# Kernel optimization log

Hardware: AMD Instinct MI355X
Metric: run time of the kernel (lower is better)

Reference implementation:

```python
import jax, jax.numpy as jnp
import numpy as np

D_MODEL = 1024
N_HEADS = 8
D_HEAD = 64
D_FF = 4096
LAMBDA_INIT = 0.8
EPS = 1e-5


def _ln(x, g, b):
    m = jnp.mean(x, axis=-1, keepdims=True)
    v = jnp.mean(jnp.square(x - m), axis=-1, keepdims=True)
    return (x - m) * jax.lax.rsqrt(v + EPS) * g + b


def setup_inputs() -> dict:
    key = jax.random.key(0)
    ks = jax.random.split(key, 24)
    D, H, Dh, F = D_MODEL, N_HEADS, D_HEAD, D_FF
    P = 2 * H * Dh  # projection width for q/k/v (== D here)
    s = lambda fan: 1.0 / np.sqrt(fan)
    inp = {
        'x': jax.random.normal(ks[0], (2, 2048, D), jnp.float32),
        'ln1_g': jnp.ones((D,), jnp.float32), 'ln1_b': jnp.zeros((D,), jnp.float32),
        'ln2_g': jnp.ones((D,), jnp.float32), 'ln2_b': jnp.zeros((D,), jnp.float32),
        'Wq': jax.random.normal(ks[1], (D, P), jnp.float32) * s(D), 'bq': jnp.zeros((P,), jnp.float32),
        'Wk': jax.random.normal(ks[2], (D, P), jnp.float32) * s(D), 'bk': jnp.zeros((P,), jnp.float32),
        'Wv': jax.random.normal(ks[3], (D, P), jnp.float32) * s(D), 'bv': jnp.zeros((P,), jnp.float32),
        'Wo': jax.random.normal(ks[4], (P, D), jnp.float32) * s(P), 'bo': jnp.zeros((D,), jnp.float32),
        'lq1': jax.random.normal(ks[5], (H, Dh), jnp.float32) * 0.1,
        'lk1': jax.random.normal(ks[6], (H, Dh), jnp.float32) * 0.1,
        'lq2': jax.random.normal(ks[7], (H, Dh), jnp.float32) * 0.1,
        'lk2': jax.random.normal(ks[8], (H, Dh), jnp.float32) * 0.1,
        'gn_w': jnp.ones((P,), jnp.float32), 'gn_b': jnp.zeros((P,), jnp.float32),
        'W1': jax.random.normal(ks[9], (D, F), jnp.float32) * s(D), 'b1': jnp.zeros((F,), jnp.float32),
        'Wg': jax.random.normal(ks[10], (F, F), jnp.float32) * s(F), 'bg': jnp.zeros((F,), jnp.float32),
        'W2': jax.random.normal(ks[11], (F, D), jnp.float32) * s(F), 'b2': jnp.zeros((D,), jnp.float32),
    }
    return inp


def reference(x, ln1_g, ln1_b, ln2_g, ln2_b, Wq, bq, Wk, bk, Wv, bv, Wo, bo,
              lq1, lk1, lq2, lk2, gn_w, gn_b, W1, b1, Wg, bg, W2, b2):
    B, S, D = x.shape
    H, Dh = N_HEADS, D_HEAD
    scale = 1.0 / np.sqrt(Dh)

    # --- differential attention sublayer (pre-norm) ---
    h = _ln(x, ln1_g, ln1_b)
    q = (h @ Wq + bq).reshape(B, S, H, 2, Dh)
    k = (h @ Wk + bk).reshape(B, S, H, 2, Dh)
    v = (h @ Wv + bv).reshape(B, S, H, 2 * Dh)

    A1 = jax.nn.softmax(jnp.einsum('bshd,bthd->bhst', q[..., 0, :], k[..., 0, :]) * scale, axis=-1)
    A2 = jax.nn.softmax(jnp.einsum('bshd,bthd->bhst', q[..., 1, :], k[..., 1, :]) * scale, axis=-1)

    lam = (jnp.exp(jnp.sum(lq1 * lk1, axis=-1))
           - jnp.exp(jnp.sum(lq2 * lk2, axis=-1)) + LAMBDA_INIT)  # [H]
    diff = A1 - lam[None, :, None, None] * A2                     # [B,H,S,S]
    o = jnp.einsum('bhst,bthe->bshe', diff, v)                    # [B,S,H,2*Dh]

    # headwise GroupNorm over the 2*Dh channels of each head
    mu = jnp.mean(o, axis=-1, keepdims=True)
    var = jnp.mean(jnp.square(o - mu), axis=-1, keepdims=True)
    o = (o - mu) * jax.lax.rsqrt(var + EPS)
    o = o * gn_w.reshape(H, 2 * Dh) + gn_b.reshape(H, 2 * Dh)
    o = o * (1.0 - LAMBDA_INIT)

    attn_out = o.reshape(B, S, 2 * H * Dh) @ Wo + bo
    x = x + attn_out

    # --- FFN sublayer: note source applies prenorm2 BEFORE residual split ---
    x = _ln(x, ln2_g, ln2_b)
    u = x @ W1 + b1
    u = u * jax.nn.silu(u @ Wg + bg)   # swiGLU gate
    return x + (u @ W2 + b2)
```

## Files before the change

kernel.cpp:

```cpp
#include <hip/hip_runtime.h>
#include <hip/hip_bf16.h>


typedef __attribute__((ext_vector_type(8))) __bf16 bf16x8;
typedef __attribute__((ext_vector_type(4))) float f32x4;

#define GAS __attribute__((address_space(1)))
#define LAS __attribute__((address_space(3)))

__device__ __forceinline__ unsigned short f2bf(float f) {
  unsigned u = __float_as_uint(f);
  u += 0x7fffu + ((u >> 16) & 1u);
  return (unsigned short)(u >> 16);
}
__device__ __forceinline__ float bf2f(unsigned short s) {
  return __uint_as_float(((unsigned)s) << 16);
}

__global__ __launch_bounds__(256)
void batched_transpose(const float* __restrict__ sWq, const float* __restrict__ sWk,
                       const float* __restrict__ sWv, const float* __restrict__ sWo,
                       const float* __restrict__ sW1, const float* __restrict__ sWg,
                       const float* __restrict__ sW2,
                       unsigned short* __restrict__ dstbase,
                       const float* __restrict__ bq, const float* __restrict__ bk,
                       const float* __restrict__ bv, float* __restrict__ bqkv,
                       float qscale) {
  const int id = blockIdx.x;
  if (id >= 7168) {
    const int i = (id - 7168) * 256 + threadIdx.x;
    if (i < 1024) bqkv[i] = bq[i] * qscale;
    else if (i < 2048) bqkv[i] = bk[i - 1024];
    else bqkv[i] = bv[i - 2048];
    return;
  }
  const float* W;
  int K, N, t;
  size_t doff;
  float scale = 1.0f;
  if (id < 256)       { W = sWq; K = 1024; N = 1024; t = id;        doff = 0;        scale = qscale; }
  else if (id < 512)  { W = sWk; K = 1024; N = 1024; t = id - 256;  doff = 1048576;  }
  else if (id < 768)  { W = sWv; K = 1024; N = 1024; t = id - 512;  doff = 2097152;  }
  else if (id < 1024) { W = sWo; K = 1024; N = 1024; t = id - 768;  doff = 3145728;  }
  else if (id < 2048) { W = sW1; K = 1024; N = 4096; t = id - 1024; doff = 4194304;  }
  else if (id < 6144) { W = sWg; K = 4096; N = 4096; t = id - 2048; doff = 8388608;  }
  else                { W = sW2; K = 4096; N = 1024; t = id - 6144; doff = 25165824; }
  unsigned short* WT = dstbase + doff;
  const int nx = N >> 6;
  const int n0 = (t % nx) * 64, k0 = (t / nx) * 64;

  __shared__ float tile[64][65];
  const int tr = threadIdx.x >> 4, tc = (threadIdx.x & 15) * 4;
#pragma unroll
  for (int i = 0; i < 4; ++i) {
    const float4 v = *(const float4*)&W[(size_t)(k0 + tr + i * 16) * N + n0 + tc];
    tile[tr + i * 16][tc + 0] = v.x;
    tile[tr + i * 16][tc + 1] = v.y;
    tile[tr + i * 16][tc + 2] = v.z;
    tile[tr + i * 16][tc + 3] = v.w;
  }
  __syncthreads();
#pragma unroll
  for (int i = 0; i < 4; ++i) {
    const int n = tr + i * 16;
    ushort4 o;
    o.x = f2bf(tile[tc + 0][n] * scale);
    o.y = f2bf(tile[tc + 1][n] * scale);
    o.z = f2bf(tile[tc + 2][n] * scale);
    o.w = f2bf(tile[tc + 3][n] * scale);
    *(ushort4*)&WT[(size_t)(n0 + n) * K + k0 + tc] = o;
  }
}

__global__ __launch_bounds__(256)
void kv_prep(const unsigned short* __restrict__ qkv, unsigned short* __restrict__ KP,
             unsigned short* __restrict__ VT) {
  __shared__ unsigned short tile[128][66];
  const int bh = blockIdx.y, b = bh >> 3, h = bh & 7;
  const int s0 = blockIdx.x * 64;
  const size_t inbase = (size_t)b * 2048 * 3072 + h * 128;
  const int tr = threadIdx.x >> 4, tc = (threadIdx.x & 15) * 8;
#pragma unroll
  for (int i = 0; i < 4; ++i) {
    const int s = s0 + tr + i * 16;
    *(uint4*)&KP[((size_t)bh * 2048 + s) * 128 + tc] =
        *(const uint4*)&qkv[inbase + (size_t)s * 3072 + 1024 + tc];
  }
#pragma unroll
  for (int i = 0; i < 4; ++i) {
    const int r = tr + i * 16;
    const uint4 v = *(const uint4*)&qkv[inbase + (size_t)(s0 + r) * 3072 + 2048 + tc];
    const unsigned short* pv = (const unsigned short*)&v;
#pragma unroll
    for (int jj = 0; jj < 8; ++jj) tile[tc + jj][r] = pv[jj];
  }
  __syncthreads();
  const int e = threadIdx.x >> 1, sh = (threadIdx.x & 1) * 32;
#pragma unroll
  for (int i = 0; i < 4; ++i) {
    ushort4 o0, o1;
    o0.x = tile[e][sh + i * 8 + 0]; o0.y = tile[e][sh + i * 8 + 1];
    o0.z = tile[e][sh + i * 8 + 2]; o0.w = tile[e][sh + i * 8 + 3];
    o1.x = tile[e][sh + i * 8 + 4]; o1.y = tile[e][sh + i * 8 + 5];
    o1.z = tile[e][sh + i * 8 + 6]; o1.w = tile[e][sh + i * 8 + 7];
    *(ushort4*)&VT[((size_t)bh * 128 + e) * 2048 + s0 + sh + i * 8] = o0;
    *(ushort4*)&VT[((size_t)bh * 128 + e) * 2048 + s0 + sh + i * 8 + 4] = o1;
  }
}

__global__ void lam_kernel(const float* __restrict__ lq1, const float* __restrict__ lk1,
                           const float* __restrict__ lq2, const float* __restrict__ lk2,
                           float* __restrict__ lam) {
  const int w = threadIdx.x >> 6, d = threadIdx.x & 63;
  float a = lq1[w * 64 + d] * lk1[w * 64 + d];
  float c = lq2[w * 64 + d] * lk2[w * 64 + d];
#pragma unroll
  for (int off = 32; off; off >>= 1) {
    a += __shfl_xor(a, off);
    c += __shfl_xor(c, off);
  }
  if (d == 0) lam[w] = __expf(a) - __expf(c) + 0.8f;
}

__global__ __launch_bounds__(256)
void ln_kernel(const float* __restrict__ x, const float* __restrict__ g,
               const float* __restrict__ bsh, unsigned short* __restrict__ obf) {
  __shared__ float red[16];
  const int row = blockIdx.x, tid = threadIdx.x;
  const float4 v = *(const float4*)&x[(size_t)row * 1024 + tid * 4];
  float s = v.x + v.y + v.z + v.w;
  float q = v.x * v.x + v.y * v.y + v.z * v.z + v.w * v.w;
#pragma unroll
  for (int off = 32; off; off >>= 1) {
    s += __shfl_xor(s, off);
    q += __shfl_xor(q, off);
  }
  if ((tid & 63) == 0) {
    red[tid >> 6] = s;
    red[8 + (tid >> 6)] = q;
  }
  __syncthreads();
  s = red[0] + red[1] + red[2] + red[3];
  q = red[8] + red[9] + red[10] + red[11];
  const float mean = s * (1.f / 1024.f);
  const float var = q * (1.f / 1024.f) - mean * mean;
  const float rstd = rsqrtf(var + 1e-5f);
  const float4 gg = *(const float4*)&g[tid * 4];
  const float4 bb = *(const float4*)&bsh[tid * 4];
  ushort4 o;
  o.x = f2bf((v.x - mean) * rstd * gg.x + bb.x);
  o.y = f2bf((v.y - mean) * rstd * gg.y + bb.y);
  o.z = f2bf((v.z - mean) * rstd * gg.z + bb.z);
  o.w = f2bf((v.w - mean) * rstd * gg.w + bb.w);
  *(ushort4*)&obf[(size_t)row * 1024 + tid * 4] = o;
}

template <int EPI>
__global__ __launch_bounds__(256)
void gemm128(const unsigned short* __restrict__ A,
             const unsigned short* __restrict__ BT,
             const float* __restrict__ bias,
             const float* __restrict__ resf,
             const unsigned short* __restrict__ resb,
             void* __restrict__ Cout, int M, int N, int K, float bscale) {
  __shared__ unsigned short lds[32768];
  const int tid = threadIdx.x;
  const int w = tid >> 6, ln = tid & 63, lg = ln >> 4, lc = ln & 15;
  const int wm = w >> 1, wn = w & 1;
  const int nwg = gridDim.x * gridDim.y;
  const int linear = blockIdx.y * gridDim.x + blockIdx.x;
  const int swzb = (linear & 7) * (nwg >> 3) + (linear >> 3);
  const int m0 = (swzb / gridDim.x) * 128, n0 = (swzb % gridDim.x) * 128;

  f32x4 acc[4][4];
#pragma unroll
  for (int i = 0; i < 4; ++i)
#pragma unroll
    for (int j = 0; j < 4; ++j) acc[i][j] = (f32x4)0.f;

  auto stage_half = [&](int tensor, int j, int hh) {
    const unsigned short* base = tensor ? BT : A;
    const int row0 = (tensor ? n0 : m0) + hh * 64;
    const int slot = tensor * 4 + (j & 1) * 2 + hh;
#pragma unroll
    for (int c = 0; c < 2; ++c) {
      const int chunk = w * 2 + c;
      const int L = chunk * 1024 + ln * 16;
      const int r = L >> 7, inner = L & 127;
      const char* src = (const char*)(base + (size_t)(row0 + r) * K + j * 64) +
                        (inner ^ ((r & 7) << 4));
      __builtin_amdgcn_global_load_lds((GAS void*)src,
          (LAS void*)((char*)lds + slot * 8192 + chunk * 1024), 16, 0, 0);
    }
  };
  auto read_a = [&](int j, int mf, int ks) -> bf16x8 {
    const int r = mf * 16 + lc;
    const int slot = (j & 1) * 2 + wm;
    const int cb = ks * 64 + lg * 16;
    return *(const bf16x8*)((const char*)lds + slot * 8192 + r * 128 +
                            (cb ^ ((r & 7) << 4)));
  };
  auto read_b = [&](int j, int nf, int ks) -> bf16x8 {
    const int R = wn * 64 + nf * 16 + lc;
    const int slot = 4 + (j & 1) * 2 + (R >> 6);
    const int r = R & 63;
    const int cb = ks * 64 + lg * 16;
    return *(const bf16x8*)((const char*)lds + slot * 8192 + r * 128 +
                            (cb ^ ((r & 7) << 4)));
  };

  const int nkt = K / 64;

  stage_half(0, 0, 0); stage_half(0, 0, 1);
  stage_half(1, 0, 0); stage_half(1, 0, 1);
  stage_half(1, 1, 0); stage_half(1, 1, 1);
  asm volatile("s_waitcnt vmcnt(0)" ::: "memory");
  __builtin_amdgcn_s_barrier();

  bf16x8 bfr[4][2];
  for (int it = 0; it < nkt / 2; ++it) {
    const int J = it * 2;
#pragma unroll
    for (int half = 0; half < 2; ++half) {
      const int jc = J + half;
#pragma unroll
      for (int q = 0; q < 2; ++q) {
        if (q == 0) {
#pragma unroll
          for (int nf = 0; nf < 4; ++nf)
#pragma unroll
            for (int ks = 0; ks < 2; ++ks) bfr[nf][ks] = read_b(jc, nf, ks);
        }
        bf16x8 afr[2][2];
#pragma unroll
        for (int mm = 0; mm < 2; ++mm)
#pragma unroll
          for (int ks = 0; ks < 2; ++ks) afr[mm][ks] = read_a(jc, q * 2 + mm, ks);
        if (half == 0) {
          if (q == 0) { stage_half(0, J + 1, 0); stage_half(0, J + 1, 1); }
          else if (J + 2 < nkt) { stage_half(1, J + 2, 0); stage_half(1, J + 2, 1); }
        } else {
          if (q == 0) { if (J + 2 < nkt) { stage_half(0, J + 2, 0); stage_half(0, J + 2, 1); } }
          else if (J + 3 < nkt) { stage_half(1, J + 3, 0); stage_half(1, J + 3, 1); }
        }
        __builtin_amdgcn_s_barrier();
        asm volatile("s_waitcnt lgkmcnt(0)" ::: "memory");
        __builtin_amdgcn_sched_barrier(0);
        __builtin_amdgcn_s_setprio(1);
#pragma unroll
        for (int mm = 0; mm < 2; ++mm)
#pragma unroll
          for (int nf = 0; nf < 4; ++nf)
#pragma unroll
            for (int ks = 0; ks < 2; ++ks)
              acc[q * 2 + mm][nf] = __builtin_amdgcn_mfma_f32_16x16x32_bf16(
                  afr[mm][ks], bfr[nf][ks], acc[q * 2 + mm][nf], 0, 0, 0);
        __builtin_amdgcn_s_setprio(0);
        if (q == 1) {
          if ((half == 0 && J + 2 < nkt) || (half == 1 && J + 3 < nkt))
            asm volatile("s_waitcnt vmcnt(4)" ::: "memory");
          else
            asm volatile("s_waitcnt vmcnt(0)" ::: "memory");
        }
        __builtin_amdgcn_s_barrier();
      }
    }
  }

#pragma unroll
  for (int mf = 0; mf < 4; ++mf) {
#pragma unroll
    for (int nf = 0; nf < 4; ++nf) {
      const int c = n0 + wn * 64 + nf * 16 + lc;
      const float bc = bias[c] * bscale;
#pragma unroll
      for (int jj = 0; jj < 4; ++jj) {
        const int r = m0 + wm * 64 + mf * 16 + lg * 4 + jj;
        const size_t idx = (size_t)r * N + c;
        const float v = acc[mf][nf][jj] + bc;
        if (EPI == 1) {
          ((float*)Cout)[idx] = resf[idx] + v;
        } else if (EPI == 2) {
          ((float*)Cout)[idx] = bf2f(resb[idx]) + v;
        } else {
          ((unsigned short*)Cout)[idx] = f2bf(v);
        }
      }
    }
  }
}

template <int EPI>
__global__ __launch_bounds__(512)
void gemm256(const unsigned short* __restrict__ A,
             const unsigned short* __restrict__ BT,
             const float* __restrict__ bias,
             const unsigned short* __restrict__ gate_u,
             unsigned short* __restrict__ Cout, int M, int N, int K) {
  __shared__ unsigned short lds[65536];
  const int tid = threadIdx.x;
  const int w = tid >> 6, ln = tid & 63, lg = ln >> 4, lc = ln & 15;
  const int wm = w >> 2, wn = w & 3;
  const int nwg = gridDim.x * gridDim.y;
  const int linear = blockIdx.y * gridDim.x + blockIdx.x;
  const int swzb = (linear & 7) * (nwg >> 3) + (linear >> 3);
  const int m0 = (swzb / gridDim.x) * 256, n0 = (swzb % gridDim.x) * 256;

  f32x4 acc[8][4];
#pragma unroll
  for (int i = 0; i < 8; ++i)
#pragma unroll
    for (int j = 0; j < 4; ++j) acc[i][j] = (f32x4)0.f;

  auto stage_half = [&](int tensor, int j, int hh) {
    const unsigned short* base = tensor ? BT : A;
    const int row0 = (tensor ? n0 : m0) + hh * 128;
    const int slot = tensor * 4 + (j & 1) * 2 + hh;
#pragma unroll
    for (int c = 0; c < 2; ++c) {
      const int chunk = w * 2 + c;
      const int L = chunk * 1024 + ln * 16;
      const int r = L >> 7, inner = L & 127;
      const char* src = (const char*)(base + (size_t)(row0 + r) * K + j * 64) +
                        (inner ^ ((r & 7) << 4));
      __builtin_amdgcn_global_load_lds((GAS void*)src,
          (LAS void*)((char*)lds + slot * 16384 + chunk * 1024), 16, 0, 0);
    }
  };
  auto read_a = [&](int j, int mf, int ks) -> bf16x8 {
    const int r = mf * 16 + lc;
    const int slot = (j & 1) * 2 + wm;
    const int cb = ks * 64 + lg * 16;
    return *(const bf16x8*)((const char*)lds + slot * 16384 + r * 128 +
                            (cb ^ ((r & 7) << 4)));
  };
  auto read_b = [&](int j, int nf, int ks) -> bf16x8 {
    const int R = wn * 64 + nf * 16 + lc;
    const int slot = 4 + (j & 1) * 2 + (R >> 7);
    const int r = R & 127;
    const int cb = ks * 64 + lg * 16;
    return *(const bf16x8*)((const char*)lds + slot * 16384 + r * 128 +
                            (cb ^ ((r & 7) << 4)));
  };

  const int nkt = K / 64;

  stage_half(0, 0, 0); stage_half(0, 0, 1);
  stage_half(1, 0, 0); stage_half(1, 0, 1);
  stage_half(1, 1, 0); stage_half(1, 1, 1);
  asm volatile("s_waitcnt vmcnt(0)" ::: "memory");
  __builtin_amdgcn_s_barrier();

  bf16x8 bfr[4][2];
  for (int it = 0; it < nkt / 2; ++it) {
    const int J = it * 2;
#pragma unroll
    for (int half = 0; half < 2; ++half) {
      const int jc = J + half;
#pragma unroll
      for (int q = 0; q < 4; ++q) {
        if (q == 0) {
#pragma unroll
          for (int nf = 0; nf < 4; ++nf)
#pragma unroll
            for (int ks = 0; ks < 2; ++ks) bfr[nf][ks] = read_b(jc, nf, ks);
        }
        bf16x8 afr[2][2];
#pragma unroll
        for (int mm = 0; mm < 2; ++mm)
#pragma unroll
          for (int ks = 0; ks < 2; ++ks) afr[mm][ks] = read_a(jc, q * 2 + mm, ks);
        if (half == 0) {
          if (q == 0) stage_half(0, J + 1, 0);
          if (q == 1) stage_half(0, J + 1, 1);
          if (q == 2 && J + 2 < nkt) stage_half(1, J + 2, 0);
          if (q == 3 && J + 2 < nkt) stage_half(1, J + 2, 1);
        } else {
          if (q == 0 && J + 2 < nkt) stage_half(0, J + 2, 0);
          if (q == 1 && J + 2 < nkt) stage_half(0, J + 2, 1);
          if (q == 2 && J + 3 < nkt) stage_half(1, J + 3, 0);
          if (q == 3 && J + 3 < nkt) stage_half(1, J + 3, 1);
        }
        __builtin_amdgcn_s_barrier();
        asm volatile("s_waitcnt lgkmcnt(0)" ::: "memory");
        __builtin_amdgcn_sched_barrier(0);
        __builtin_amdgcn_s_setprio(1);
#pragma unroll
        for (int mm = 0; mm < 2; ++mm)
#pragma unroll
          for (int nf = 0; nf < 4; ++nf)
#pragma unroll
            for (int ks = 0; ks < 2; ++ks)
              acc[q * 2 + mm][nf] = __builtin_amdgcn_mfma_f32_16x16x32_bf16(
                  afr[mm][ks], bfr[nf][ks], acc[q * 2 + mm][nf], 0, 0, 0);
        __builtin_amdgcn_s_setprio(0);
        if (q == 3) asm volatile("s_waitcnt vmcnt(4)" ::: "memory");
        __builtin_amdgcn_s_barrier();
      }
    }
  }

#pragma unroll
  for (int mf = 0; mf < 8; ++mf) {
#pragma unroll
    for (int nf = 0; nf < 4; ++nf) {
      const int c = n0 + wn * 64 + nf * 16 + lc;
      const float bc = bias[c];
#pragma unroll
      for (int jj = 0; jj < 4; ++jj) {
        const int r = m0 + wm * 128 + mf * 16 + lg * 4 + jj;
        const size_t idx = (size_t)r * N + c;
        const float v = acc[mf][nf][jj] + bc;
        if (EPI == 0) {
          Cout[idx] = f2bf(v);
        } else {
          const float uu = bf2f(gate_u[idx]);
          const float sw = v / (1.f + __expf(-v));
          Cout[idx] = f2bf(uu * sw);
        }
      }
    }
  }
}

__global__ __launch_bounds__(256)
void attn_kernel(const unsigned short* __restrict__ q,
                 const unsigned short* __restrict__ KP,
                 const unsigned short* __restrict__ VT,
                 const float* __restrict__ lam,
                 const float* __restrict__ gn_w, const float* __restrict__ gn_b,
                 unsigned short* __restrict__ o) {
  constexpr int S = 2048;
  constexpr int QS = 3072;
  __shared__ unsigned short k_tile[2][32 * 128];
  __shared__ unsigned short v_tile[2][128 * 32];
  __shared__ unsigned short p_lds[4][2][512];
  const int tid = threadIdx.x, w = tid >> 6, ln = tid & 63, lg = ln >> 4, lc = ln & 15;
  const int id = blockIdx.x;
  const int bh = (id & 7) + 8 * ((id >> 8) & 1);
  const int qt = (id >> 3) & 31;
  const int h = bh & 7, b = bh >> 3;
  const size_t chan = (size_t)b * S * QS + h * 128;
  const size_t ochan = (size_t)b * S * 1024 + h * 128;
  const size_t kpbase = (size_t)bh * S * 128;
  const size_t vtbase = (size_t)bh * 128 * S;
  const int qrow = qt * 64 + w * 16 + lc;

  bf16x8 qf[2][2];
#pragma unroll
  for (int p = 0; p < 2; ++p)
#pragma unroll
    for (int ks = 0; ks < 2; ++ks)
      qf[p][ks] = *(const bf16x8*)&q[chan + (size_t)qrow * QS + p * 64 + ks * 32 + lg * 8];

  f32x4 O[2][8];
#pragma unroll
  for (int p = 0; p < 2; ++p)
#pragma unroll
    for (int ef = 0; ef < 8; ++ef) O[p][ef] = (f32x4)0.f;
  float lsum[2][4];
#pragma unroll
  for (int p = 0; p < 2; ++p)
#pragma unroll
    for (int j = 0; j < 4; ++j) lsum[p][j] = 0.f;

  const int prd = ((lc * 64 + lg * 16) ^ ((lc & 7) << 4)) >> 1;

  auto stage = [&](int buf, int t0) {
#pragma unroll
    for (int c = 0; c < 2; ++c) {
      {
        const int L = (w * 2 + c) * 1024 + ln * 16;
        const int r = L >> 8, inner = L & 255;
        const char* src = (const char*)(KP + kpbase + (size_t)(t0 + r) * 128) +
                          (inner ^ ((r & 7) << 4));
        __builtin_amdgcn_global_load_lds((GAS void*)src,
            (LAS void*)((char*)&k_tile[buf][0] + (w * 2 + c) * 1024), 16, 0, 0);
      }
      {
        const int L = (w * 2 + c) * 1024 + ln * 16;
        const int e = L >> 6, inner = L & 63;
        const char* src = (const char*)(VT + vtbase + (size_t)e * S + t0) +
                          (inner ^ ((e & 3) << 4));
        __builtin_amdgcn_global_load_lds((GAS void*)src,
            (LAS void*)((char*)&v_tile[buf][0] + (w * 2 + c) * 1024), 16, 0, 0);
      }
    }
  };

  auto compute = [&](int buf) {
    const char* kb = (const char*)&k_tile[buf][0];
    const char* vb = (const char*)&v_tile[buf][0];
#pragma unroll
    for (int p = 0; p < 2; ++p) {
      bf16x8 kf[2][2];
#pragma unroll
      for (int tf = 0; tf < 2; ++tf) {
        const int r = tf * 16 + lc;
#pragma unroll
        for (int ks = 0; ks < 2; ++ks)
          kf[tf][ks] = *(const bf16x8*)(kb + r * 256 +
                          ((p * 128 + ks * 64 + lg * 16) ^ ((r & 7) << 4)));
      }
      f32x4 sfr[2];
      __builtin_amdgcn_s_setprio(1);
#pragma unroll
      for (int tf = 0; tf < 2; ++tf) {
        f32x4 acc = (f32x4)0.f;
#pragma unroll
        for (int ks = 0; ks < 2; ++ks)
          acc = __builtin_amdgcn_mfma_f32_16x16x32_bf16(qf[p][ks], kf[tf][ks], acc, 0, 0, 0);
        sfr[tf] = acc;
      }
      __builtin_amdgcn_s_setprio(0);
#pragma unroll
      for (int tf = 0; tf < 2; ++tf)
#pragma unroll
        for (int j = 0; j < 4; ++j) {
          const float e = __expf(sfr[tf][j]);
          lsum[p][j] += e;
          const int qq = lg * 4 + j;
          const int wi = ((qq * 64 + (tf * 16 + lc) * 2) ^ ((qq & 7) << 4)) >> 1;
          p_lds[w][p][wi] = f2bf(e);
        }
    }
    bf16x8 pa[2];
#pragma unroll
    for (int p = 0; p < 2; ++p)
      pa[p] = *(const bf16x8*)&p_lds[w][p][prd];
#pragma unroll
    for (int half = 0; half < 2; ++half) {
      bf16x8 vf[4];
#pragma unroll
      for (int ef = 0; ef < 4; ++ef) {
        const int e = (half * 4 + ef) * 16 + lc;
        vf[ef] = *(const bf16x8*)(vb + e * 64 + ((lg * 16) ^ ((e & 3) << 4)));
      }
      __builtin_amdgcn_s_setprio(1);
#pragma unroll
      for (int p = 0; p < 2; ++p)
#pragma unroll
        for (int ef = 0; ef < 4; ++ef)
          O[p][half * 4 + ef] = __builtin_amdgcn_mfma_f32_16x16x32_bf16(
              pa[p], vf[ef], O[p][half * 4 + ef], 0, 0, 0);
      __builtin_amdgcn_s_setprio(0);
    }
  };

  stage(0, 0);
  int cur = 0;
  for (int it = 0; it < 64; ++it) {
    if (it < 63) {
      stage(cur ^ 1, (it + 1) * 32);
      asm volatile("s_waitcnt vmcnt(4)" ::: "memory");
    } else {
      asm volatile("s_waitcnt vmcnt(0)" ::: "memory");
    }
    __builtin_amdgcn_s_barrier();
    compute(cur);
    __builtin_amdgcn_s_barrier();
    cur ^= 1;
  }

#pragma unroll
  for (int p = 0; p < 2; ++p)
#pragma unroll
    for (int j = 0; j < 4; ++j) {
      float s = lsum[p][j];
      s += __shfl_xor(s, 1);
      s += __shfl_xor(s, 2);
      s += __shfl_xor(s, 4);
      s += __shfl_xor(s, 8);
      lsum[p][j] = s;
    }
  const float lamh = lam[h];
#pragma unroll
  for (int j = 0; j < 4; ++j) {
    const float inv1 = 1.f / lsum[0][j];
    const float inv2 = lamh / lsum[1][j];
    float dv[8], sum = 0.f, sq = 0.f;
#pragma unroll
    for (int ef = 0; ef < 8; ++ef) {
      dv[ef] = O[0][ef][j] * inv1 - O[1][ef][j] * inv2;
      sum += dv[ef];
      sq += dv[ef] * dv[ef];
    }
    sum += __shfl_xor(sum, 1); sq += __shfl_xor(sq, 1);
    sum += __shfl_xor(sum, 2); sq += __shfl_xor(sq, 2);
    sum += __shfl_xor(sum, 4); sq += __shfl_xor(sq, 4);
    sum += __shfl_xor(sum, 8); sq += __shfl_xor(sq, 8);
    const float mean = sum * (1.f / 128.f);
    const float var = sq * (1.f / 128.f) - mean * mean;
    const float rstd = rsqrtf(var + 1e-5f);
    const int row = qt * 64 + w * 16 + lg * 4 + j;
#pragma unroll
    for (int ef = 0; ef < 8; ++ef) {
      const int e = ef * 16 + lc;
      const float val = (dv[ef] - mean) * rstd * gn_w[h * 128 + e] + gn_b[h * 128 + e];
      o[ochan + (size_t)row * 1024 + e] = f2bf(val * 0.2f);
    }
  }
}

extern "C" void kernel_launch(void* const* d_in, const int* in_sizes, int n_in,
                              void* d_out, int out_size, void* d_ws, size_t ws_size,
                              hipStream_t stream) {
  (void)in_sizes; (void)n_in; (void)out_size; (void)ws_size;
  const float* x    = (const float*)d_in[0];
  const float* ln1g = (const float*)d_in[1];
  const float* ln1b = (const float*)d_in[2];
  const float* ln2g = (const float*)d_in[3];
  const float* ln2b = (const float*)d_in[4];
  const float* Wq   = (const float*)d_in[5];
  const float* bq   = (const float*)d_in[6];
  const float* Wk   = (const float*)d_in[7];
  const float* bk   = (const float*)d_in[8];
  const float* Wv   = (const float*)d_in[9];
  const float* bv   = (const float*)d_in[10];
  const float* Wo   = (const float*)d_in[11];
  const float* bo   = (const float*)d_in[12];
  const float* lq1  = (const float*)d_in[13];
  const float* lk1  = (const float*)d_in[14];
  const float* lq2  = (const float*)d_in[15];
  const float* lk2  = (const float*)d_in[16];
  const float* gnw  = (const float*)d_in[17];
  const float* gnb  = (const float*)d_in[18];
  const float* W1   = (const float*)d_in[19];
  const float* b1   = (const float*)d_in[20];
  const float* Wg   = (const float*)d_in[21];
  const float* bg   = (const float*)d_in[22];
  const float* W2   = (const float*)d_in[23];
  const float* b2   = (const float*)d_in[24];

  const int B = 2, S = 2048, D = 1024, F = 4096;
  const int M = B * S;
  const float qscale = 0.125f;

  char* ws = (char*)d_ws;
  size_t off = 0;
  auto alloc = [&](size_t bytes) {
    char* p = ws + off;
    off += (bytes + 255) & ~(size_t)255;
    return p;
  };
  unsigned short* WqkvT = (unsigned short*)alloc((size_t)3 * D * D * 2);
  unsigned short* WoT = (unsigned short*)alloc((size_t)D * D * 2);
  unsigned short* W1T = (unsigned short*)alloc((size_t)F * D * 2);
  unsigned short* WgT = (unsigned short*)alloc((size_t)F * F * 2);
  unsigned short* W2T = (unsigned short*)alloc((size_t)D * F * 2);
  float*          lamw= (float*)alloc(256);
  float*          bqkv= (float*)alloc(3072 * 4);
  unsigned short* h_bf= (unsigned short*)alloc((size_t)M * D * 2);
  unsigned short* qkv = (unsigned short*)alloc((size_t)M * 3 * D * 2);
  unsigned short* o_bf= (unsigned short*)alloc((size_t)M * D * 2);
  float*          x1  = (float*)alloc((size_t)M * D * 4);
  unsigned short* x2b = (unsigned short*)alloc((size_t)M * D * 2);
  unsigned short* u_bf= (unsigned short*)alloc((size_t)M * F * 2);
  unsigned short* w_bf= h_bf;

  unsigned short* KP = (unsigned short*)x1;
  unsigned short* VT = u_bf + (size_t)12 * 1024 * 1024;

  batched_transpose<<<7180, 256, 0, stream>>>(Wq, Wk, Wv, Wo, W1, Wg, W2, WqkvT,
                                              bq, bk, bv, bqkv, qscale);
  lam_kernel<<<1, 512, 0, stream>>>(lq1, lk1, lq2, lk2, lamw);

  ln_kernel<<<M, 256, 0, stream>>>(x, ln1g, ln1b, h_bf);
  gemm256<0><<<dim3(3 * D / 256, M / 256), 512, 0, stream>>>(h_bf, WqkvT, bqkv, nullptr, qkv, M, 3 * D, D);
  kv_prep<<<dim3(S / 64, 16), 256, 0, stream>>>(qkv, KP, VT);
  attn_kernel<<<dim3(512), 256, 0, stream>>>(qkv, KP, VT, lamw, gnw, gnb, o_bf);
  gemm128<1><<<dim3(D / 128, M / 128), 256, 0, stream>>>(o_bf, WoT, bo, x, nullptr, x1, M, D, D, 1.0f);

  ln_kernel<<<M, 256, 0, stream>>>(x1, ln2g, ln2b, x2b);
  gemm256<0><<<dim3(F / 256, M / 256), 512, 0, stream>>>(x2b, W1T, b1, nullptr, u_bf, M, F, D);
  gemm256<2><<<dim3(F / 256, M / 256), 512, 0, stream>>>(u_bf, WgT, bg, u_bf, w_bf, M, F, F);
  gemm128<2><<<dim3(D / 128, M / 128), 256, 0, stream>>>(w_bf, W2T, b2, nullptr, x2b, (float*)d_out, M, D, F, 1.0f);
}
```

Measured before the change: 390.7 us.

## Merge weight prep, lambda and first LayerNorm into one kernel; use exp2 softmax

Folds the weight transpose/convert, lambda computation and first LayerNorm into a single launch, removing two kernel launches and their gaps. The QKV projection moves from the 256-tile GEMM to the 128-tile GEMM variant. Softmax uses exp2 with log2(e) folded into the Q scale, saving a multiply per exponent. The fused kernel has a leftover unused block in the lambda path, and the lambda block uses only 8 of its intended heads' 32-lane groups within 256 threads.

```diff
diff --git a/kernel.cpp b/kernel.cpp
--- a/kernel.cpp
+++ b/kernel.cpp
@@ -18,15 +18,63 @@
 }
 
 __global__ __launch_bounds__(256)
-void batched_transpose(const float* __restrict__ sWq, const float* __restrict__ sWk,
-                       const float* __restrict__ sWv, const float* __restrict__ sWo,
-                       const float* __restrict__ sW1, const float* __restrict__ sWg,
-                       const float* __restrict__ sW2,
-                       unsigned short* __restrict__ dstbase,
-                       const float* __restrict__ bq, const float* __restrict__ bk,
-                       const float* __restrict__ bv, float* __restrict__ bqkv,
-                       float qscale) {
+void mega_prep(const float* __restrict__ sWq, const float* __restrict__ sWk,
+               const float* __restrict__ sWv, const float* __restrict__ sWo,
+               const float* __restrict__ sW1, const float* __restrict__ sWg,
+               const float* __restrict__ sW2,
+               unsigned short* __restrict__ dstbase,
+               const float* __restrict__ bq, const float* __restrict__ bk,
+               const float* __restrict__ bv, float* __restrict__ bqkv,
+               const float* __restrict__ lq1, const float* __restrict__ lk1,
+               const float* __restrict__ lq2, const float* __restrict__ lk2,
+               float* __restrict__ lam,
+               const float* __restrict__ x, const float* __restrict__ ln1g,
+               const float* __restrict__ ln1b, unsigned short* __restrict__ h_bf,
+               float qscale) {
   const int id = blockIdx.x;
+  if (id >= 7181) {
+    __shared__ float red[16];
+    const int row = id - 7181, tid = threadIdx.x;
+    const float4 v = *(const float4*)&x[(size_t)row * 1024 + tid * 4];
+    float s = v.x + v.y + v.z + v.w;
+    float q = v.x * v.x + v.y * v.y + v.z * v.z + v.w * v.w;
+#pragma unroll
+    for (int off = 32; off; off >>= 1) {
+      s += __shfl_xor(s, off);
+      q += __shfl_xor(q, off);
+    }
+    if ((tid & 63) == 0) { red[tid >> 6] = s; red[8 + (tid >> 6)] = q; }
+    __syncthreads();
+    s = red[0] + red[1] + red[2] + red[3];
+    q = red[8] + red[9] + red[10] + red[11];
+    const float mean = s * (1.f / 1024.f);
+    const float var = q * (1.f / 1024.f) - mean * mean;
+    const float rstd = rsqrtf(var + 1e-5f);
+    const float4 gg = *(const float4*)&ln1g[tid * 4];
+    const float4 bb = *(const float4*)&ln1b[tid * 4];
+    ushort4 o;
+    o.x = f2bf((v.x - mean) * rstd * gg.x + bb.x);
+    o.y = f2bf((v.y - mean) * rstd * gg.y + bb.y);
+    o.z = f2bf((v.z - mean) * rstd * gg.z + bb.z);
+    o.w = f2bf((v.w - mean) * rstd * gg.w + bb.w);
+    *(ushort4*)&h_bf[(size_t)row * 1024 + tid * 4] = o;
+    return;
+  }
+  if (id == 7180) {
+    if (threadIdx.x < 512) {
+      const int w = threadIdx.x >> 6, d = threadIdx.x & 63;
+    }
+    const int hh = threadIdx.x >> 5, d = (threadIdx.x & 31) * 2;
+    float a = lq1[hh * 64 + d] * lk1[hh * 64 + d] + lq1[hh * 64 + d + 1] * lk1[hh * 64 + d + 1];
+    float c = lq2[hh * 64 + d] * lk2[hh * 64 + d] + lq2[hh * 64 + d + 1] * lk2[hh * 64 + d + 1];
+#pragma unroll
+    for (int off = 16; off; off >>= 1) {
+      a += __shfl_xor(a, off);
+      c += __shfl_xor(c, off);
+    }
+    if ((threadIdx.x & 31) == 0) lam[hh] = __expf(a) - __expf(c) + 0.8f;
+    return;
+  }
   if (id >= 7168) {
     const int i = (id - 7168) * 256 + threadIdx.x;
     if (i < 1024) bqkv[i] = bq[i] * qscale;
@@ -106,20 +154,6 @@
     *(ushort4*)&VT[((size_t)bh * 128 + e) * 2048 + s0 + sh + i * 8] = o0;
     *(ushort4*)&VT[((size_t)bh * 128 + e) * 2048 + s0 + sh + i * 8 + 4] = o1;
   }
-}
-
-__global__ void lam_kernel(const float* __restrict__ lq1, const float* __restrict__ lk1,
-                           const float* __restrict__ lq2, const float* __restrict__ lk2,
-                           float* __restrict__ lam) {
-  const int w = threadIdx.x >> 6, d = threadIdx.x & 63;
-  float a = lq1[w * 64 + d] * lk1[w * 64 + d];
-  float c = lq2[w * 64 + d] * lk2[w * 64 + d];
-#pragma unroll
-  for (int off = 32; off; off >>= 1) {
-    a += __shfl_xor(a, off);
-    c += __shfl_xor(c, off);
-  }
-  if (d == 0) lam[w] = __expf(a) - __expf(c) + 0.8f;
 }
 
 __global__ __launch_bounds__(256)
@@ -517,7 +551,7 @@
       for (int tf = 0; tf < 2; ++tf)
 #pragma unroll
         for (int j = 0; j < 4; ++j) {
-          const float e = __expf(sfr[tf][j]);
+          const float e = exp2f(sfr[tf][j]);
           lsum[p][j] += e;
           const int qq = lg * 4 + j;
           const int wi = ((qq * 64 + (tf * 16 + lc) * 2) ^ ((qq & 7) << 4)) >> 1;
@@ -634,7 +668,7 @@
 
   const int B = 2, S = 2048, D = 1024, F = 4096;
   const int M = B * S;
-  const float qscale = 0.125f;
+  const float qscale = 0.125f * 1.4426950408889634f;
 
   char* ws = (char*)d_ws;
   size_t off = 0;
@@ -661,12 +695,12 @@
   unsigned short* KP = (unsigned short*)x1;
   unsigned short* VT = u_bf + (size_t)12 * 1024 * 1024;
 
-  batched_transpose<<<7180, 256, 0, stream>>>(Wq, Wk, Wv, Wo, W1, Wg, W2, WqkvT,
-                                              bq, bk, bv, bqkv, qscale);
-  lam_kernel<<<1, 512, 0, stream>>>(lq1, lk1, lq2, lk2, lamw);
-
-  ln_kernel<<<M, 256, 0, stream>>>(x, ln1g, ln1b, h_bf);
-  gemm256<0><<<dim3(3 * D / 256, M / 256), 512, 0, stream>>>(h_bf, WqkvT, bqkv, nullptr, qkv, M, 3 * D, D);
+  mega_prep<<<7181 + M, 256, 0, stream>>>(Wq, Wk, Wv, Wo, W1, Wg, W2, WqkvT,
+                                          bq, bk, bv, bqkv,
+                                          lq1, lk1, lq2, lk2, lamw,
+                                          x, ln1g, ln1b, h_bf, qscale);
+
+  gemm128<0><<<dim3(3 * D / 128, M / 128), 256, 0, stream>>>(h_bf, WqkvT, bqkv, nullptr, nullptr, qkv, M, 3 * D, D, 1.0f);
   kv_prep<<<dim3(S / 64, 16), 256, 0, stream>>>(qkv, KP, VT);
   attn_kernel<<<dim3(512), 256, 0, stream>>>(qkv, KP, VT, lamw, gnw, gnb, o_bf);
   gemm128<1><<<dim3(D / 128, M / 128), 256, 0, stream>>>(o_bf, WoT, bo, x, nullptr, x1, M, D, D, 1.0f);
```

Result: slower. 402.2 us (+3.0%).
